# Performance work log

Hardware: AMD Instinct MI355X
Metric: run time of the kernel (lower is better)

## Reference

```python
import jax, jax.numpy as jnp
import numpy as np

HIDDEN_SIZE = 1024  # used for scaling, per the module's __init__
NEG_INF = -1e9

def setup_inputs() -> dict:
    key = jax.random.key(0)
    kq, kk, kv, km = jax.random.split(key, 4)
    B, H, S, D = 2, 16, 2048, 64
    query = jax.random.normal(kq, (B, H, S, D), dtype=jnp.float32)
    k_ = jax.random.normal(kk, (B, H, S, D), dtype=jnp.float32)
    v_ = jax.random.normal(kv, (B, H, S, D), dtype=jnp.float32)
    mask = jax.random.randint(km, (B, S), 0, 2, dtype=jnp.int32)
    return {"query": query, "key": k_, "value": v_, "mask": mask}

def reference(query, key, value, mask):
    # scores: [B,H,S,S]
    scores = jnp.einsum("bhqd,bhkd->bhqk", query, key)
    scores = scores / jnp.sqrt(jnp.float32(HIDDEN_SIZE))
    m = mask.astype(jnp.float32)[:, None, None, :]  # [B,1,1,S]
    scores = scores + NEG_INF * (1.0 - m)
    weights = jax.nn.softmax(scores, axis=-1)
    return jnp.einsum("bhqk,bhkd->bhqd", weights, value)
```

## Files before the change

kernel.cpp:

```cpp
#include <hip/hip_runtime.h>
#include <hip/hip_bf16.h>

typedef __bf16 bf16x8 __attribute__((ext_vector_type(8)));
typedef __bf16 bf16x4 __attribute__((ext_vector_type(4)));
typedef float  f32x4  __attribute__((ext_vector_type(4)));

constexpr int SEQ = 2048;
constexpr int HD  = 64;
constexpr int KT  = 64;
constexpr int QB  = 64;
constexpr int NT  = SEQ / KT;
constexpr int LDP = 72;

__global__ __launch_bounds__(256)
void prepass(const float* __restrict__ K, const float* __restrict__ V,
             __bf16* __restrict__ Kf, __bf16* __restrict__ Vf)
{
    __shared__ __bf16 Kt[64][72];
    __shared__ __bf16 Vt[64][72];

    const int t = blockIdx.x, bh = blockIdx.y, tid = threadIdx.x;
    const size_t base = (size_t)bh * SEQ * HD + (size_t)t * 64 * HD;

    #pragma unroll
    for (int p = 0; p < 4; ++p) {
        int idx = p * 256 + tid;
        int row = idx >> 4, c4 = (idx & 15) * 4;
        float4 kv = *(const float4*)(K + base + row * HD + c4);
        bf16x4 kb;
        kb[0]=(__bf16)kv.x; kb[1]=(__bf16)kv.y; kb[2]=(__bf16)kv.z; kb[3]=(__bf16)kv.w;
        *(bf16x4*)&Kt[row][c4] = kb;
        float4 vv = *(const float4*)(V + base + row * HD + c4);
        bf16x4 vb;
        vb[0]=(__bf16)vv.x; vb[1]=(__bf16)vv.y; vb[2]=(__bf16)vv.z; vb[3]=(__bf16)vv.w;
        *(bf16x4*)&Vt[row][c4] = vb;
    }
    __syncthreads();

    __bf16* kd = Kf + (size_t)(bh * NT + t) * 4096;
    __bf16* vd = Vf + (size_t)(bh * NT + t) * 4096;
    #pragma unroll
    for (int p = 0; p < 2; ++p) {
        int gran = p * 256 + tid;
        int frag = gran >> 6, l = gran & 63, lo = l & 15, hi = l >> 4;
        int s = frag >> 1, kh = frag & 1;
        bf16x8 ko = *(const bf16x8*)&Kt[s*16 + lo][kh*32 + hi*8];
        *(bf16x8*)(kd + gran * 8) = ko;
        bf16x8 vo;
        #pragma unroll
        for (int j = 0; j < 8; ++j)
            vo[j] = Vt[kh*32 + hi*8 + j][s*16 + lo];
        *(bf16x8*)(vd + gran * 8) = vo;
    }
}

__global__ __launch_bounds__(256, 4)
void attn_fwd3(const float* __restrict__ Q, const __bf16* __restrict__ Kf,
               const __bf16* __restrict__ Vf, const int* __restrict__ mask,
               float* __restrict__ out)
{
    __shared__ __bf16 Pl[4][16][LDP];
    __shared__ unsigned long long Ml[NT];

    const int tid = threadIdx.x;
    const int w   = tid >> 6;
    const int l   = tid & 63;
    const int lo  = l & 15;
    const int hi  = l >> 4;

    const int id   = blockIdx.x;
    const int virt = (id & 7) * 128 + (id >> 3);
    const int bh   = virt >> 5;
    const int qb   = virt & 31;
    const int b    = bh >> 4;
    const size_t base = (size_t)bh * SEQ * HD;
    const int qbase = qb * QB + w * 16;

    {
        const int4* mp = (const int4*)(mask + b * SEQ);
        int4 m0 = mp[tid * 2], m1 = mp[tid * 2 + 1];
        unsigned byte =
            ((unsigned)(m0.x != 0)     ) | ((unsigned)(m0.y != 0) << 1) |
            ((unsigned)(m0.z != 0) << 2) | ((unsigned)(m0.w != 0) << 3) |
            ((unsigned)(m1.x != 0) << 4) | ((unsigned)(m1.y != 0) << 5) |
            ((unsigned)(m1.z != 0) << 6) | ((unsigned)(m1.w != 0) << 7);
        ((unsigned char*)Ml)[tid] = (unsigned char)byte;
    }

    bf16x8 qf[2];
    {
        const float* qp = Q + base + (size_t)(qbase + lo) * HD;
        #pragma unroll
        for (int kh = 0; kh < 2; ++kh) {
            const float4 a = *(const float4*)(qp + kh*32 + hi*8);
            const float4 c = *(const float4*)(qp + kh*32 + hi*8 + 4);
            bf16x8 f;
            f[0]=(__bf16)a.x; f[1]=(__bf16)a.y; f[2]=(__bf16)a.z; f[3]=(__bf16)a.w;
            f[4]=(__bf16)c.x; f[5]=(__bf16)c.y; f[6]=(__bf16)c.z; f[7]=(__bf16)c.w;
            qf[kh] = f;
        }
    }

    __syncthreads();

    f32x4 acc[4] = {{0,0,0,0},{0,0,0,0},{0,0,0,0},{0,0,0,0}};
    float m_run  = -INFINITY;
    float l_part = 0.f;

    const __bf16* Kb = Kf + (size_t)bh * NT * 4096 + l * 8;
    const __bf16* Vb = Vf + (size_t)bh * NT * 4096 + l * 8;

    for (int t = 0; t < NT; ++t) {
        const __bf16* Kt = Kb + (size_t)t * 4096;
        const __bf16* Vt = Vb + (size_t)t * 4096;

        float sv[4][4];
        const unsigned long long mb = Ml[t];
        __builtin_amdgcn_s_setprio(1);
        #pragma unroll
        for (int s = 0; s < 4; ++s) {
            bf16x8 k0 = *(const bf16x8*)(Kt + (s*2+0) * 512);
            bf16x8 k1 = *(const bf16x8*)(Kt + (s*2+1) * 512);
            f32x4 c = {0,0,0,0};
            c = __builtin_amdgcn_mfma_f32_16x16x32_bf16(k0, qf[0], c, 0, 0, 0);
            c = __builtin_amdgcn_mfma_f32_16x16x32_bf16(k1, qf[1], c, 0, 0, 0);
            const unsigned ms = (unsigned)(mb >> (s * 16));
            #pragma unroll
            for (int r = 0; r < 4; ++r)
                sv[s][r] = c[r] * 0.03125f +
                           (((ms >> (hi*4 + r)) & 1u) ? 0.f : -1e9f);
        }
        __builtin_amdgcn_s_setprio(0);

        bf16x8 vfr[8];
        #pragma unroll
        for (int f = 0; f < 8; ++f) vfr[f] = *(const bf16x8*)(Vt + f * 512);

        float pm = sv[0][0];
        #pragma unroll
        for (int s = 0; s < 4; ++s)
            #pragma unroll
            for (int r = 0; r < 4; ++r)
                pm = fmaxf(pm, sv[s][r]);

        if (!__all(pm - m_run <= 8.0f)) {
            float pmr = pm;
            pmr = fmaxf(pmr, __shfl_xor(pmr, 16));
            pmr = fmaxf(pmr, __shfl_xor(pmr, 32));
            const float mn  = fmaxf(m_run, pmr);
            const float scl = __expf(m_run - mn);
            m_run = mn;
            l_part *= scl;
            #pragma unroll
            for (int nt = 0; nt < 4; ++nt)
                #pragma unroll
                for (int r = 0; r < 4; ++r)
                    acc[nt][r] *= scl;
        }

        float p[4][4], ls = 0.f;
        #pragma unroll
        for (int s = 0; s < 4; ++s) {
            #pragma unroll
            for (int r = 0; r < 4; ++r) {
                p[s][r] = __expf(sv[s][r] - m_run);
                ls += p[s][r];
            }
        }
        l_part += ls;

        #pragma unroll
        for (int s = 0; s < 4; ++s) {
            bf16x4 pk;
            pk[0]=(__bf16)p[s][0]; pk[1]=(__bf16)p[s][1];
            pk[2]=(__bf16)p[s][2]; pk[3]=(__bf16)p[s][3];
            *(bf16x4*)&Pl[w][lo][s*16 + hi*4] = pk;
        }

        bf16x8 pa0 = *(const bf16x8*)&Pl[w][lo][hi * 8];
        bf16x8 pa1 = *(const bf16x8*)&Pl[w][lo][32 + hi * 8];
        __builtin_amdgcn_s_setprio(1);
        #pragma unroll
        for (int nt = 0; nt < 4; ++nt) {
            acc[nt] = __builtin_amdgcn_mfma_f32_16x16x32_bf16(vfr[nt*2+0], pa0, acc[nt], 0, 0, 0);
            acc[nt] = __builtin_amdgcn_mfma_f32_16x16x32_bf16(vfr[nt*2+1], pa1, acc[nt], 0, 0, 0);
        }
        __builtin_amdgcn_s_setprio(0);
    }

    float lr = l_part;
    lr += __shfl_xor(lr, 16);
    lr += __shfl_xor(lr, 32);
    const float inv = 1.0f / lr;

    float* op = out + base + (size_t)(qbase + lo) * HD;
    #pragma unroll
    for (int nt = 0; nt < 4; ++nt)
        #pragma unroll
        for (int r = 0; r < 4; ++r)
            op[nt*16 + hi*4 + r] = acc[nt][r] * inv;
}

__global__ __launch_bounds__(256)
void attn_fwd_legacy(const float* __restrict__ Q, const float* __restrict__ K,
                     const float* __restrict__ V, const int* __restrict__ mask,
                     float* __restrict__ out)
{
    __shared__ __bf16 Kl[KT][LDP];
    __shared__ __bf16 Vl[HD][LDP];
    __shared__ __bf16 Pl[4][16][LDP];

    const int tid = threadIdx.x;
    const int w   = tid >> 6;
    const int l   = tid & 63;
    const int lo  = l & 15;
    const int hi  = l >> 4;

    const int bh = blockIdx.y;
    const int b  = bh >> 4;
    const size_t base = (size_t)bh * SEQ * HD;
    const int qbase = blockIdx.x * QB + w * 16;

    bf16x8 qf[2];
    {
        const float* qp = Q + base + (size_t)(qbase + lo) * HD;
        #pragma unroll
        for (int kh = 0; kh < 2; ++kh) {
            const float4 a = *(const float4*)(qp + kh*32 + hi*8);
            const float4 c = *(const float4*)(qp + kh*32 + hi*8 + 4);
            bf16x8 f;
            f[0]=(__bf16)a.x; f[1]=(__bf16)a.y; f[2]=(__bf16)a.z; f[3]=(__bf16)a.w;
            f[4]=(__bf16)c.x; f[5]=(__bf16)c.y; f[6]=(__bf16)c.z; f[7]=(__bf16)c.w;
            qf[kh] = f;
        }
    }

    f32x4 acc[4] = {{0,0,0,0},{0,0,0,0},{0,0,0,0},{0,0,0,0}};
    float m_run[4], l_run[4];
    #pragma unroll
    for (int r = 0; r < 4; ++r) { m_run[r] = -INFINITY; l_run[r] = 0.f; }

    const int* maskp = mask + b * SEQ;

    for (int k0 = 0; k0 < SEQ; k0 += KT) {
        #pragma unroll
        for (int i = 0; i < 4; ++i) {
            int e4 = i * 256 + tid;
            int key = e4 >> 4, d4 = (e4 & 15) * 4;
            float4 kv = *(const float4*)(K + base + (size_t)(k0 + key) * HD + d4);
            bf16x4 kb;
            kb[0]=(__bf16)kv.x; kb[1]=(__bf16)kv.y; kb[2]=(__bf16)kv.z; kb[3]=(__bf16)kv.w;
            *(bf16x4*)&Kl[key][d4] = kb;
        }
        #pragma unroll
        for (int i = 0; i < 4; ++i) {
            int e4 = i * 256 + tid;
            int key = e4 >> 4, d4 = (e4 & 15) * 4;
            float4 vv = *(const float4*)(V + base + (size_t)(k0 + key) * HD + d4);
            Vl[d4+0][key] = (__bf16)vv.x;
            Vl[d4+1][key] = (__bf16)vv.y;
            Vl[d4+2][key] = (__bf16)vv.z;
            Vl[d4+3][key] = (__bf16)vv.w;
        }
        __syncthreads();

        float sv[4][4];
        #pragma unroll
        for (int s = 0; s < 4; ++s) {
            f32x4 c = {0,0,0,0};
            bf16x8 kf0 = *(const bf16x8*)&Kl[s*16 + lo][hi*8];
            bf16x8 kf1 = *(const bf16x8*)&Kl[s*16 + lo][32 + hi*8];
            c = __builtin_amdgcn_mfma_f32_16x16x32_bf16(qf[0], kf0, c, 0, 0, 0);
            c = __builtin_amdgcn_mfma_f32_16x16x32_bf16(qf[1], kf1, c, 0, 0, 0);
            const int km = maskp[k0 + s*16 + lo];
            #pragma unroll
            for (int r = 0; r < 4; ++r)
                sv[s][r] = km ? (c[r] * 0.03125f) : -1e9f;
        }

        float tm[4];
        #pragma unroll
        for (int r = 0; r < 4; ++r)
            tm[r] = fmaxf(fmaxf(sv[0][r], sv[1][r]), fmaxf(sv[2][r], sv[3][r]));
        #pragma unroll
        for (int off = 1; off < 16; off <<= 1)
            #pragma unroll
            for (int r = 0; r < 4; ++r)
                tm[r] = fmaxf(tm[r], __shfl_xor(tm[r], off));

        float scl[4];
        #pragma unroll
        for (int r = 0; r < 4; ++r) {
            float mn = fmaxf(m_run[r], tm[r]);
            scl[r] = __expf(m_run[r] - mn);
            m_run[r] = mn;
        }
        float pv_[4][4], rs[4] = {0.f, 0.f, 0.f, 0.f};
        #pragma unroll
        for (int s = 0; s < 4; ++s)
            #pragma unroll
            for (int r = 0; r < 4; ++r) {
                float p = __expf(sv[s][r] - m_run[r]);
                pv_[s][r] = p;
                rs[r] += p;
            }
        #pragma unroll
        for (int off = 1; off < 16; off <<= 1)
            #pragma unroll
            for (int r = 0; r < 4; ++r)
                rs[r] += __shfl_xor(rs[r], off);
        #pragma unroll
        for (int r = 0; r < 4; ++r)
            l_run[r] = l_run[r] * scl[r] + rs[r];
        #pragma unroll
        for (int nt = 0; nt < 4; ++nt)
            #pragma unroll
            for (int r = 0; r < 4; ++r)
                acc[nt][r] *= scl[r];

        #pragma unroll
        for (int s = 0; s < 4; ++s)
            #pragma unroll
            for (int r = 0; r < 4; ++r)
                Pl[w][hi*4 + r][s*16 + lo] = (__bf16)pv_[s][r];

        bf16x8 pa0 = *(const bf16x8*)&Pl[w][lo][hi*8];
        bf16x8 pa1 = *(const bf16x8*)&Pl[w][lo][32 + hi*8];
        #pragma unroll
        for (int nt = 0; nt < 4; ++nt) {
            bf16x8 v0 = *(const bf16x8*)&Vl[nt*16 + lo][hi*8];
            bf16x8 v1 = *(const bf16x8*)&Vl[nt*16 + lo][32 + hi*8];
            acc[nt] = __builtin_amdgcn_mfma_f32_16x16x32_bf16(pa0, v0, acc[nt], 0, 0, 0);
            acc[nt] = __builtin_amdgcn_mfma_f32_16x16x32_bf16(pa1, v1, acc[nt], 0, 0, 0);
        }
        __syncthreads();
    }

    float inv[4];
    #pragma unroll
    for (int r = 0; r < 4; ++r) inv[r] = 1.0f / l_run[r];
    float* op = out + base + (size_t)qbase * HD;
    #pragma unroll
    for (int nt = 0; nt < 4; ++nt)
        #pragma unroll
        for (int r = 0; r < 4; ++r)
            op[(size_t)(hi*4 + r) * HD + nt*16 + lo] = acc[nt][r] * inv[r];
}

extern "C" void kernel_launch(void* const* d_in, const int* in_sizes, int n_in,
                              void* d_out, int out_size, void* d_ws, size_t ws_size,
                              hipStream_t stream) {
    (void)in_sizes; (void)n_in; (void)out_size;
    const float* Q  = (const float*)d_in[0];
    const float* K  = (const float*)d_in[1];
    const float* V  = (const float*)d_in[2];
    const int* mask = (const int*)d_in[3];
    float* out      = (float*)d_out;

    const size_t kv_elems = (size_t)32 * SEQ * HD;
    const size_t need = kv_elems * 2  * 2 ;

    if (ws_size >= need) {
        __bf16* Kf = (__bf16*)d_ws;
        __bf16* Vf = Kf + kv_elems;
        hipLaunchKernelGGL(prepass, dim3(NT, 32), dim3(256), 0, stream, K, V, Kf, Vf);
        hipLaunchKernelGGL(attn_fwd3, dim3(1024), dim3(256), 0, stream,
                           Q, Kf, Vf, mask, out);
    } else {
        hipLaunchKernelGGL(attn_fwd_legacy, dim3(SEQ / QB, 32), dim3(256), 0, stream,
                           Q, K, V, mask, out);
    }
}
```

Baseline: 161.2 us.

## Stage K/V tiles into double-buffered LDS via async global-to-LDS loads

Replaces per-wave direct global loads of the pre-packed K and V tiles with block-wide global_load_lds transfers into two LDS buffers, prefetching the next tile while computing the current one. This removes four-fold redundant global/L2 traffic across waves and overlaps load latency with MFMA work. It adds a block barrier each iteration and more LDS usage, and lowers the launch-bounds occupancy hint from 4 to 3 blocks per CU.

```diff
diff --git a/kernel.cpp b/kernel.cpp
--- a/kernel.cpp
+++ b/kernel.cpp
@@ -4,6 +4,9 @@
 typedef __bf16 bf16x8 __attribute__((ext_vector_type(8)));
 typedef __bf16 bf16x4 __attribute__((ext_vector_type(4)));
 typedef float  f32x4  __attribute__((ext_vector_type(4)));
+
+typedef __attribute__((address_space(3))) void lds_void;
+typedef __attribute__((address_space(1))) const void gbl_void;
 
 constexpr int SEQ = 2048;
 constexpr int HD  = 64;
@@ -54,11 +57,13 @@
     }
 }
 
-__global__ __launch_bounds__(256, 4)
-void attn_fwd3(const float* __restrict__ Q, const __bf16* __restrict__ Kf,
+__global__ __launch_bounds__(256, 3)
+void attn_fwd4(const float* __restrict__ Q, const __bf16* __restrict__ Kf,
                const __bf16* __restrict__ Vf, const int* __restrict__ mask,
                float* __restrict__ out)
 {
+    __shared__ __bf16 Kl[2][4096];
+    __shared__ __bf16 Vl[2][4096];
     __shared__ __bf16 Pl[4][16][LDP];
     __shared__ unsigned long long Ml[NT];
 
@@ -101,26 +106,41 @@
         }
     }
 
-    __syncthreads();
+    const __bf16* Ksrc = Kf + (size_t)bh * NT * 4096;
+    const __bf16* Vsrc = Vf + (size_t)bh * NT * 4096;
+
+    auto stage = [&](int buf, int t) {
+        const __bf16* kg = Ksrc + (size_t)t * 4096;
+        const __bf16* vg = Vsrc + (size_t)t * 4096;
+        #pragma unroll
+        for (int r = 0; r < 2; ++r) {
+            __builtin_amdgcn_global_load_lds(
+                (gbl_void*)(kg + (size_t)(r*256 + tid) * 8),
+                (lds_void*)(&Kl[buf][0] + (r*256 + w*64) * 8), 16, 0, 0);
+            __builtin_amdgcn_global_load_lds(
+                (gbl_void*)(vg + (size_t)(r*256 + tid) * 8),
+                (lds_void*)(&Vl[buf][0] + (r*256 + w*64) * 8), 16, 0, 0);
+        }
+    };
 
     f32x4 acc[4] = {{0,0,0,0},{0,0,0,0},{0,0,0,0},{0,0,0,0}};
     float m_run  = -INFINITY;
     float l_part = 0.f;
 
-    const __bf16* Kb = Kf + (size_t)bh * NT * 4096 + l * 8;
-    const __bf16* Vb = Vf + (size_t)bh * NT * 4096 + l * 8;
+    stage(0, 0);
+    __syncthreads();
 
     for (int t = 0; t < NT; ++t) {
-        const __bf16* Kt = Kb + (size_t)t * 4096;
-        const __bf16* Vt = Vb + (size_t)t * 4096;
+        const int buf = t & 1;
+        if (t + 1 < NT) stage(buf ^ 1, t + 1);
 
         float sv[4][4];
         const unsigned long long mb = Ml[t];
         __builtin_amdgcn_s_setprio(1);
         #pragma unroll
         for (int s = 0; s < 4; ++s) {
-            bf16x8 k0 = *(const bf16x8*)(Kt + (s*2+0) * 512);
-            bf16x8 k1 = *(const bf16x8*)(Kt + (s*2+1) * 512);
+            bf16x8 k0 = *(const bf16x8*)&Kl[buf][(s*2+0) * 512 + l*8];
+            bf16x8 k1 = *(const bf16x8*)&Kl[buf][(s*2+1) * 512 + l*8];
             f32x4 c = {0,0,0,0};
             c = __builtin_amdgcn_mfma_f32_16x16x32_bf16(k0, qf[0], c, 0, 0, 0);
             c = __builtin_amdgcn_mfma_f32_16x16x32_bf16(k1, qf[1], c, 0, 0, 0);
@@ -134,7 +154,8 @@
 
         bf16x8 vfr[8];
         #pragma unroll
-        for (int f = 0; f < 8; ++f) vfr[f] = *(const bf16x8*)(Vt + f * 512);
+        for (int f = 0; f < 8; ++f)
+            vfr[f] = *(const bf16x8*)&Vl[buf][f * 512 + l*8];
 
         float pm = sv[0][0];
         #pragma unroll
@@ -186,6 +207,8 @@
             acc[nt] = __builtin_amdgcn_mfma_f32_16x16x32_bf16(vfr[nt*2+1], pa1, acc[nt], 0, 0, 0);
         }
         __builtin_amdgcn_s_setprio(0);
+
+        __syncthreads();
     }
 
     float lr = l_part;
@@ -364,7 +387,7 @@
         __bf16* Kf = (__bf16*)d_ws;
         __bf16* Vf = Kf + kv_elems;
         hipLaunchKernelGGL(prepass, dim3(NT, 32), dim3(256), 0, stream, K, V, Kf, Vf);
-        hipLaunchKernelGGL(attn_fwd3, dim3(1024), dim3(256), 0, stream,
+        hipLaunchKernelGGL(attn_fwd4, dim3(1024), dim3(256), 0, stream,
                            Q, Kf, Vf, mask, out);
     } else {
         hipLaunchKernelGGL(attn_fwd_legacy, dim3(SEQ / QB, 32), dim3(256), 0, stream,
```

Result: slower. 165.2 us (+2.5%).
